# Kernel optimization log

Hardware: AMD Instinct MI355X
Metric: run time of the kernel (lower is better)

The kernel has to match this reference:

```python
import jax, jax.numpy as jnp
from jax import lax
import numpy as np

EPS = 1e-5


def ref_points(Hk, Wk):
    # torch linspace(0.5, Hk-0.5, Hk)/Hk * 2 - 1, stacked (y, x)
    ys = (jnp.linspace(0.5, Hk - 0.5, Hk) / Hk) * 2.0 - 1.0
    xs = (jnp.linspace(0.5, Wk - 0.5, Wk) / Wk) * 2.0 - 1.0
    yy, xx = jnp.meshgrid(ys, xs, indexing='ij')
    return jnp.stack([yy, xx], axis=-1)  # (Hk, Wk, 2) in (y, x) order


def grid_sample(img, grid):
    # Bilinear, align_corners=True, zeros padding (torch F.grid_sample defaults).
    # img: (N, C, Hi, Wi); grid: (N, Hg, Wg, 2) with (x, y) in [-1, 1].
    N, C, Hi, Wi = img.shape
    Hg, Wg = grid.shape[1], grid.shape[2]
    gx = (grid[..., 0] + 1.0) * 0.5 * (Wi - 1)
    gy = (grid[..., 1] + 1.0) * 0.5 * (Hi - 1)
    x0 = jnp.floor(gx)
    y0 = jnp.floor(gy)
    wx1 = gx - x0
    wy1 = gy - y0
    imgf = img.reshape(N, C, Hi * Wi)

    def corner(ix, iy, w):
        valid = (ix >= 0) & (ix < Wi) & (iy >= 0) & (iy < Hi)
        idx = (jnp.clip(iy, 0, Hi - 1).astype(jnp.int32) * Wi
               + jnp.clip(ix, 0, Wi - 1).astype(jnp.int32)).reshape(N, -1)
        vals = jax.vmap(lambda im, f: im[:, f])(imgf, idx)  # (N, C, Hg*Wg)
        return vals * (w * valid).reshape(N, 1, -1)

    out = (corner(x0, y0, (1 - wx1) * (1 - wy1))
           + corner(x0 + 1, y0, wx1 * (1 - wy1))
           + corner(x0, y0 + 1, (1 - wx1) * wy1)
           + corner(x0 + 1, y0 + 1, wx1 * wy1))
    return out.reshape(N, C, Hg, Wg)


def setup_inputs() -> dict:
    key = jax.random.key(0)
    ks = jax.random.split(key, 8)
    B, C, H, W = 8, 128, 64, 64
    gc, nH = 64, 4
    return {
        'x': jax.random.normal(ks[0], (B, C, H, W), jnp.float32),
        'w_dw': jax.random.normal(ks[1], (gc, 1, 5, 5), jnp.float32) * 0.1,
        'ln_w': jnp.ones((gc,), jnp.float32),
        'w_off': jax.random.normal(ks[2], (3, gc), jnp.float32) * 0.1,
        'wq': jax.random.normal(ks[3], (C, C), jnp.float32) * 0.05,
        'wk': jax.random.normal(ks[4], (C, C), jnp.float32) * 0.05,
        'wv': jax.random.normal(ks[5], (C, C), jnp.float32) * 0.05,
        'wo': jax.random.normal(ks[6], (C, C), jnp.float32) * 0.05,
        'rpe': jax.random.normal(ks[7], (nH, 2 * H - 1, 2 * W - 1), jnp.float32) * 0.01,
    }


def reference(x, w_dw, ln_w, w_off, wq, wk, wv, wo, rpe):
    B, C, H, W = x.shape
    G, nH = 2, 4
    gc = C // G           # group channels
    dh = C // nH          # head channels
    gh = nH // G          # heads per group
    scale = dh ** -0.5
    orf = 1.0             # offset_range_factor

    conv1x1 = lambda t, w: jnp.einsum('oi,bihw->bohw', w, t)

    q = conv1x1(x, wq)                                    # (B, C, H, W)
    q_off = q.reshape(B * G, gc, H, W)

    # conv_offset: depthwise 5x5 stride 4 pad 2 -> BiasFree LN (over C) -> GELU -> 1x1 to 3
    off = lax.conv_general_dilated(q_off, w_dw, (4, 4), ((2, 2), (2, 2)),
                                   dimension_numbers=('NCHW', 'OIHW', 'NCHW'),
                                   feature_group_count=gc)  # (B*G, gc, Hk, Wk)
    var = jnp.var(off, axis=1, keepdims=True)
    off = off / jnp.sqrt(var + EPS) * ln_w.reshape(1, -1, 1, 1)
    off = jax.nn.gelu(off, approximate=False)
    off = jnp.einsum('oi,bihw->bohw', w_off, off)          # (B*G, 3, Hk, Wk)

    Hk, Wk = off.shape[2], off.shape[3]
    n = Hk * Wk

    # channel 0 = y offset, channel 1 = x offset, channel 2 = modulation
    offset = jnp.stack([jnp.tanh(off[:, 0]) * (orf / Hk),
                        jnp.tanh(off[:, 1]) * (orf / Wk)], axis=-1)  # (B*G, Hk, Wk, 2) (y,x)
    dm = jax.nn.sigmoid(off[:, 2])[:, None]                # (B*G, 1, Hk, Wk)

    pos = offset + ref_points(Hk, Wk)[None]                # (B*G, Hk, Wk, 2) (y,x)

    xs = grid_sample(x.reshape(B * G, gc, H, W), pos[..., ::-1])  # grid in (x,y)
    xs = (xs * dm).reshape(B, C, 1, n)

    k = conv1x1(xs, wk).reshape(B * nH, dh, n)
    v = conv1x1(xs, wv).reshape(B * nH, dh, n)
    qf = q.reshape(B * nH, dh, H * W)

    attn = jnp.einsum('bcm,bcn->bmn', qf, k) * scale       # (B*nH, H*W, n)

    # relative-position bias sampled at continuous displacements
    rpe_b = jnp.broadcast_to(rpe[None], (B, nH, 2 * H - 1, 2 * W - 1)
                             ).reshape(B * G, gh, 2 * H - 1, 2 * W - 1)
    qg = ref_points(H, W).reshape(H * W, 2)                # (H*W, 2)
    disp = (qg[None, :, None, :] - pos.reshape(B * G, 1, n, 2)) * 0.5  # (B*G, H*W, n, 2)
    bias = grid_sample(rpe_b, disp[..., ::-1]).reshape(B * nH, H * W, n)

    attn = jax.nn.softmax(attn + bias, axis=2)
    out = jnp.einsum('bmn,bcn->bcm', attn, v).reshape(B, C, H, W)
    return conv1x1(out, wo)
```

## Files before the change

### kernel.cpp

```cpp
#include <hip/hip_runtime.h>
#include <hip/hip_bf16.h>
#include <math.h>

#define HW 4096
#define NCH 128

typedef __attribute__((ext_vector_type(8))) short short8;
typedef __attribute__((ext_vector_type(4))) float f32x4;

__device__ __forceinline__ short f2bf(float f) {
  union { __hip_bfloat16 h; short s; } u;
  u.h = __float2bfloat16(f);
  return u.s;
}
__device__ __forceinline__ float bf2f(short s) {
  union { unsigned u; float f; } u;
  u.u = ((unsigned)(unsigned short)s) << 16;
  return u.f;
}

__global__ __launch_bounds__(256) void xq_kernel(
    const float* __restrict__ x, const float* __restrict__ wq,
    short* __restrict__ xT, float* __restrict__ qT, short* __restrict__ qbf) {
  __shared__ float s[128][33];
  int tid = threadIdx.x;
  int b = blockIdx.y;
  int m0 = blockIdx.x * 32;
  {
    int ml = tid & 31, c0 = tid >> 5;
#pragma unroll
    for (int i = 0; i < 16; ++i) {
      int c = i * 8 + c0;
      s[c][ml] = x[((size_t)(b * NCH + c)) * HW + m0 + ml];
    }
  }
  __syncthreads();
  {
    int c = tid & 127, mh = tid >> 7;
#pragma unroll
    for (int i = 0; i < 16; ++i) {
      int m = i * 2 + mh;
      xT[((size_t)(b * HW + m0 + m)) * NCH + c] = f2bf(s[c][m]);
    }
  }
  int w = tid >> 6, lane = tid & 63, l15 = lane & 15, qd = lane >> 4;
  int mt = w & 1, og = w >> 1;
  int mrow = mt * 16 + l15;
  f32x4 acc[4];
#pragma unroll
  for (int oi = 0; oi < 4; ++oi) acc[oi] = (f32x4){0.f, 0.f, 0.f, 0.f};
#pragma unroll
  for (int kc = 0; kc < 4; ++kc) {
    short8 ah, al;
#pragma unroll
    for (int j = 0; j < 8; ++j) {
      float v = s[kc * 32 + qd * 8 + j][mrow];
      short hi = f2bf(v);
      ah[j] = hi;
      al[j] = f2bf(v - bf2f(hi));
    }
#pragma unroll
    for (int oi = 0; oi < 4; ++oi) {
      const float* wr =
          wq + (size_t)((og * 4 + oi) * 16 + l15) * NCH + kc * 32 + qd * 8;
      f32x4 w0 = *(const f32x4*)wr;
      f32x4 w1 = *(const f32x4*)(wr + 4);
      short8 bh, bl;
#pragma unroll
      for (int j = 0; j < 4; ++j) {
        short h0 = f2bf(w0[j]);
        bh[j] = h0;
        bl[j] = f2bf(w0[j] - bf2f(h0));
        short h1 = f2bf(w1[j]);
        bh[4 + j] = h1;
        bl[4 + j] = f2bf(w1[j] - bf2f(h1));
      }
      acc[oi] = __builtin_amdgcn_mfma_f32_16x16x32_bf16(ah, bh, acc[oi], 0, 0, 0);
      acc[oi] = __builtin_amdgcn_mfma_f32_16x16x32_bf16(al, bh, acc[oi], 0, 0, 0);
      acc[oi] = __builtin_amdgcn_mfma_f32_16x16x32_bf16(ah, bl, acc[oi], 0, 0, 0);
    }
  }
#pragma unroll
  for (int oi = 0; oi < 4; ++oi)
#pragma unroll
    for (int r = 0; r < 4; ++r) {
      size_t idx = ((size_t)(b * HW + m0 + mt * 16 + qd * 4 + r)) * NCH +
                   og * 64 + oi * 16 + l15;
      qT[idx] = acc[oi][r];
      qbf[idx] = f2bf(acc[oi][r]);
    }
}

__device__ __forceinline__ float wsum64(float v) {
#pragma unroll
  for (int o = 32; o > 0; o >>= 1) v += __shfl_xor(v, o);
  return v;
}

__global__ __launch_bounds__(256) void conv_offset_kernel(
    const float* __restrict__ qT, const float* __restrict__ w_dw,
    const float* __restrict__ ln_w, const float* __restrict__ w_off,
    const float* __restrict__ wk, const float* __restrict__ wv,
    const float* __restrict__ wo, const float* __restrict__ rpe,
    float* __restrict__ pos, float* __restrict__ dm,
    short* __restrict__ wk_bf, short* __restrict__ wv_bf,
    short* __restrict__ wo_bf, unsigned* __restrict__ tab) {
  int tid = threadIdx.x;
  if (blockIdx.x >= 64) {
    int id = (blockIdx.x - 64) * 16 + blockIdx.y;
    if (id < 64) {
      int i = id * 256 + tid;
      wk_bf[i] = f2bf(wk[i]);
      wv_bf[i] = f2bf(wv[i]);
      wo_bf[i] = f2bf(wo[i]);
    } else {
      int i = (id - 64) * 256 + tid;
      int h = i >> 14, r = i & 16383;
      int row = r >> 7, col = r & 127;
      float lo = 0.f, hi = 0.f;
      if (col < 127) {
        if (row >= 1) lo = rpe[h * 16129 + (row - 1) * 127 + col];
        if (row < 127) hi = rpe[h * 16129 + row * 127 + col];
      }
      union { unsigned u; _Float16 h2[2]; } pk;
      pk.h2[0] = (_Float16)lo;
      pk.h2[1] = (_Float16)hi;
      tab[i] = pk.u;
    }
    return;
  }
  int c = tid & 63;
  int p = blockIdx.x * 4 + (tid >> 6);
  int bg = blockIdx.y;
  int py = p >> 4, px = p & 15;
  const float* qp = qT + (size_t)(bg >> 1) * HW * NCH + (bg & 1) * 64 + c;
  const float* wd = w_dw + c * 25;
  float acc = 0.f;
#pragma unroll
  for (int ky = 0; ky < 5; ++ky) {
    int iy = 4 * py + ky - 2;
    if (iy < 0 || iy >= 64) continue;
#pragma unroll
    for (int kx = 0; kx < 5; ++kx) {
      int ix = 4 * px + kx - 2;
      if (ix < 0 || ix >= 64) continue;
      acc += wd[ky * 5 + kx] * qp[(size_t)(iy * 64 + ix) * NCH];
    }
  }
  float mean = wsum64(acc) * (1.f / 64.f);
  float msq = wsum64(acc * acc) * (1.f / 64.f);
  float var = msq - mean * mean;
  float g = acc * rsqrtf(var + 1e-5f) * ln_w[c];
  g = 0.5f * g * (1.f + erff(g * 0.70710678118654752f));
  float o0 = wsum64(w_off[c] * g);
  float o1 = wsum64(w_off[64 + c] * g);
  float o2 = wsum64(w_off[128 + c] * g);
  if (c == 0) {
    int idx = bg * 256 + p;
    pos[idx * 2] = tanhf(o0) * (1.f / 16.f) + ((py + 0.5f) * (1.f / 8.f) - 1.f);
    pos[idx * 2 + 1] = tanhf(o1) * (1.f / 16.f) + ((px + 0.5f) * (1.f / 8.f) - 1.f);
    dm[idx] = 1.f / (1.f + expf(-o2));
  }
}

__global__ __launch_bounds__(256) void sample_xs_kernel(
    const short* __restrict__ xT, const float* __restrict__ pos,
    const float* __restrict__ dm, short* __restrict__ xsT) {
  int tid = threadIdx.x;
  int c = tid & 63;
  int p = blockIdx.y * 4 + (tid >> 6);
  int bg = blockIdx.x;
  int b = bg >> 1, ch0 = (bg & 1) * 64;
  int idx = bg * 256 + p;
  float posy = pos[idx * 2], posx = pos[idx * 2 + 1];
  float dmv = dm[idx];
  float gx = (posx + 1.f) * 31.5f;
  float gy = (posy + 1.f) * 31.5f;
  float x0f = floorf(gx), y0f = floorf(gy);
  int ix = (int)x0f, iy = (int)y0f;
  float fx = gx - x0f, fy = gy - y0f;
  float w00 = (1.f - fx) * (1.f - fy), w10 = fx * (1.f - fy);
  float w01 = (1.f - fx) * fy, w11 = fx * fy;
  bool vx0 = (ix >= 0 && ix < 64), vx1 = (ix + 1 >= 0 && ix + 1 < 64);
  bool vy0 = (iy >= 0 && iy < 64), vy1 = (iy + 1 >= 0 && iy + 1 < 64);
  if (!(vx0 && vy0)) w00 = 0.f;
  if (!(vx1 && vy0)) w10 = 0.f;
  if (!(vx0 && vy1)) w01 = 0.f;
  if (!(vx1 && vy1)) w11 = 0.f;
  int x0c = min(max(ix, 0), 63), x1c = min(max(ix + 1, 0), 63);
  int y0c = min(max(iy, 0), 63), y1c = min(max(iy + 1, 0), 63);
  size_t rb = (size_t)b * HW * NCH + ch0 + c;
  float v = w00 * bf2f(xT[rb + (size_t)(y0c * 64 + x0c) * NCH]) +
            w10 * bf2f(xT[rb + (size_t)(y0c * 64 + x1c) * NCH]) +
            w01 * bf2f(xT[rb + (size_t)(y1c * 64 + x0c) * NCH]) +
            w11 * bf2f(xT[rb + (size_t)(y1c * 64 + x1c) * NCH]);
  xsT[((size_t)(b * 256 + p)) * NCH + ch0 + c] = f2bf(v * dmv);
}

__global__ __launch_bounds__(256) void kv_mfma_kernel(
    const short* __restrict__ xsT, const short* __restrict__ wk_bf,
    const short* __restrict__ wv_bf, short* __restrict__ kbf,
    short* __restrict__ vbf) {
  int tid = threadIdx.x;
  int w = tid >> 6, lane = tid & 63, l15 = lane & 15, qd = lane >> 4;
  int bh = blockIdx.x, b = bh >> 2;
  int n0 = blockIdx.y * 64 + w * 16;
  int ot = blockIdx.z & 1;
  f32x4 acc = (f32x4){0.f, 0.f, 0.f, 0.f};

  size_t xrow = ((size_t)(b * 256 + n0 + l15)) * NCH + qd * 8;
  size_t wrow = (size_t)((bh & 3) * 32 + ot * 16 + l15) * NCH + qd * 8;
  if ((blockIdx.z & 2) == 0) {
#pragma unroll
    for (int kc = 0; kc < 4; ++kc) {
      short8 a = *(const short8*)&xsT[xrow + kc * 32];
      short8 bb = *(const short8*)&wk_bf[wrow + kc * 32];
      acc = __builtin_amdgcn_mfma_f32_16x16x32_bf16(a, bb, acc, 0, 0, 0);
    }
#pragma unroll
    for (int r = 0; r < 4; ++r)
      kbf[((size_t)(bh * 256 + n0 + qd * 4 + r)) * 32 + ot * 16 + l15] =
          f2bf(acc[r]);
  } else {
#pragma unroll
    for (int kc = 0; kc < 4; ++kc) {
      short8 bb = *(const short8*)&xsT[xrow + kc * 32];
      short8 a = *(const short8*)&wv_bf[wrow + kc * 32];
      acc = __builtin_amdgcn_mfma_f32_16x16x32_bf16(a, bb, acc, 0, 0, 0);
    }
#pragma unroll
    for (int r = 0; r < 4; ++r)
      vbf[((size_t)(bh * 32 + ot * 16 + qd * 4 + r)) * 256 + n0 + l15] =
          f2bf(acc[r]);
  }
}

#define PROW 264
#define TROWS 72

__global__ __launch_bounds__(256) void attn_kernel(
    const short* __restrict__ qbf, const short* __restrict__ kbf,
    const short* __restrict__ vbf, const float* __restrict__ pos,
    const unsigned* __restrict__ tabg, short* __restrict__ outT) {
  __shared__ __align__(16) unsigned s_tab[TROWS * 128];
  __shared__ __align__(16) float s_pos[512];
  short* s_p = (short*)s_tab;

  int tid = threadIdx.x;
  int wv = tid >> 6;
  int lane = tid & 63;
  int l15 = lane & 15;
  int qd = lane >> 4;
  int bh = blockIdx.y;
  int b = bh >> 2, h = bh & 3;
  int bg = b * 2 + (h >> 1);
  int m0 = blockIdx.x * 64 + wv * 16;

  float ry = ((float)blockIdx.x + 0.5f) * (1.f / 32.f) - 1.f;
  float gy0 = 63.f + ry * 31.5f;
  int row0 = min(max((int)floorf(gy0) - 34, 0), 128 - TROWS);

  {
    const uint4* src = (const uint4*)(tabg + (size_t)h * 16384 + row0 * 128);
    uint4* dst = (uint4*)s_tab;
#pragma unroll
    for (int i = 0; i < 9; ++i) dst[i * 256 + tid] = src[i * 256 + tid];
    const float* posg = pos + (size_t)bg * 512;
    s_pos[tid] = posg[tid];
    s_pos[256 + tid] = posg[256 + tid];
  }

  short8 qfrag =
      *(const short8*)&qbf[((size_t)(b * HW + m0 + l15)) * NCH + h * 32 + qd * 8];

  f32x4 acc[16];
  {
    const short* kb = kbf + ((size_t)bh * 256 + l15) * 32 + qd * 8;
#pragma unroll
    for (int t = 0; t < 16; ++t) {
      short8 kf = *(const short8*)(kb + t * 16 * 32);
      acc[t] = __builtin_amdgcn_mfma_f32_16x16x32_bf16(
          kf, qfrag, (f32x4){0.f, 0.f, 0.f, 0.f}, 0, 0, 0);
    }
  }
  __syncthreads();

  int m = m0 + l15;
  float gx0 = ((((float)(m & 63) + 0.5f) * (1.f / 32.f) - 1.f) * 0.5f + 1.f) * 63.f;
  float gyb = gy0 - (float)row0 + 1.f;
  float mxA[4] = {-1e30f, -1e30f, -1e30f, -1e30f};
#pragma unroll
  for (int t = 0; t < 16; ++t) {
    const f32x4* pp4 = (const f32x4*)&s_pos[(t * 16 + qd * 4) * 2];
    f32x4 pA = pp4[0];
    f32x4 pB = pp4[1];
    float py[4] = {pA[0], pA[2], pB[0], pB[2]};
    float px[4] = {pA[1], pA[3], pB[1], pB[3]};
#pragma unroll
    for (int r = 0; r < 4; ++r) {
      float gy = gyb - py[r] * 31.5f;
      float gx = gx0 - px[r] * 31.5f;
      float y0f = floorf(gy), x0f = floorf(gx);
      float fy = gy - y0f, fx = gx - x0f;
      int row = (int)y0f << 7;
      int xl = (int)x0f;
      unsigned left = s_tab[row + (xl & 127)];
      unsigned right = s_tab[row + xl + 1];
      union { unsigned u; _Float16 h2[2]; } L, R;
      L.u = left;
      R.u = right;
      float t00 = (float)L.h2[0], t01 = (float)L.h2[1];
      float t10 = (float)R.h2[0], t11 = (float)R.h2[1];
      float r0 = t00 + fx * (t10 - t00);
      float r1 = t01 + fx * (t11 - t01);
      float bias = r0 + fy * (r1 - r0);
      float s = fmaf(acc[t][r], 0.17677669529663688f, bias);
      acc[t][r] = s;
      mxA[r] = fmaxf(mxA[r], s);
    }
  }
  float mx = fmaxf(fmaxf(mxA[0], mxA[1]), fmaxf(mxA[2], mxA[3]));
  mx = fmaxf(mx, __shfl_xor(mx, 16));
  float M = fmaxf(mx, __shfl_xor(mx, 32));

  float smA[4] = {0.f, 0.f, 0.f, 0.f};
#pragma unroll
  for (int t = 0; t < 16; ++t) {
#pragma unroll
    for (int r = 0; r < 4; ++r) {
      float e = __expf(acc[t][r] - M);
      acc[t][r] = e;
      smA[r] += e;
    }
  }
  float sm = (smA[0] + smA[1]) + (smA[2] + smA[3]);
  sm += __shfl_xor(sm, 16);
  sm += __shfl_xor(sm, 32);
  float inv = 1.f / sm;

  __syncthreads();

  {
    short* pw = s_p + wv * 16 * PROW + l15 * PROW;
#pragma unroll
    for (int t = 0; t < 16; ++t) {
      int n = t * 16 + qd * 4;
      short4 pk;
      pk.x = f2bf(acc[t][0]);
      pk.y = f2bf(acc[t][1]);
      pk.z = f2bf(acc[t][2]);
      pk.w = f2bf(acc[t][3]);
      *(short4*)(pw + n) = pk;
    }
  }

  f32x4 o0 = {0.f, 0.f, 0.f, 0.f}, o1 = {0.f, 0.f, 0.f, 0.f};
  {
    const short* vb = vbf + ((size_t)bh * 32 + l15) * 256 + qd * 8;
    const short* pr = s_p + wv * 16 * PROW + l15 * PROW + qd * 8;
#pragma unroll
    for (int ch = 0; ch < 8; ++ch) {
      short8 pf = *(const short8*)(pr + ch * 32);
      short8 v0 = *(const short8*)(vb + ch * 32);
      short8 v1 = *(const short8*)(vb + 16 * 256 + ch * 32);
      o0 = __builtin_amdgcn_mfma_f32_16x16x32_bf16(v0, pf, o0, 0, 0, 0);
      o1 = __builtin_amdgcn_mfma_f32_16x16x32_bf16(v1, pf, o1, 0, 0, 0);
    }
  }
  {
    size_t row = (size_t)(b * HW + m0 + l15) * NCH + h * 32 + qd * 4;
    short4 s0, s1;
    s0.x = f2bf(o0[0] * inv); s0.y = f2bf(o0[1] * inv);
    s0.z = f2bf(o0[2] * inv); s0.w = f2bf(o0[3] * inv);
    s1.x = f2bf(o1[0] * inv); s1.y = f2bf(o1[1] * inv);
    s1.z = f2bf(o1[2] * inv); s1.w = f2bf(o1[3] * inv);
    *(short4*)&outT[row] = s0;
    *(short4*)&outT[row + 16] = s1;
  }
}

__global__ __launch_bounds__(256) void wo_mfma_kernel(
    const short* __restrict__ attnT, const short* __restrict__ wo_bf,
    float* __restrict__ out) {
  int tid = threadIdx.x;
  int wv = tid >> 6;
  int lane = tid & 63;
  int l15 = lane & 15;
  int qd = lane >> 4;
  int b = blockIdx.x >> 6;
  int m0 = (blockIdx.x & 63) * 64 + wv * 16;

  f32x4 acc[8];
#pragma unroll
  for (int ot = 0; ot < 8; ++ot) acc[ot] = (f32x4){0.f, 0.f, 0.f, 0.f};

  const short* arow = attnT + (size_t)(b * HW + m0 + l15) * NCH + qd * 8;
  const short* wrow = wo_bf + (size_t)l15 * NCH + qd * 8;
#pragma unroll
  for (int kc = 0; kc < 4; ++kc) {
    short8 afrag = *(const short8*)(arow + kc * 32);
#pragma unroll
    for (int ot = 0; ot < 8; ++ot) {
      short8 bfrag = *(const short8*)(wrow + (size_t)ot * 16 * NCH + kc * 32);
      acc[ot] = __builtin_amdgcn_mfma_f32_16x16x32_bf16(afrag, bfrag, acc[ot],
                                                        0, 0, 0);
    }
  }
#pragma unroll
  for (int ot = 0; ot < 8; ++ot) {
    float* op = out + ((size_t)b * NCH + ot * 16 + l15) * HW + m0 + qd * 4;
    *(f32x4*)op = acc[ot];
  }
}

extern "C" void kernel_launch(void* const* d_in, const int* in_sizes, int n_in,
                              void* d_out, int out_size, void* d_ws,
                              size_t ws_size, hipStream_t stream) {
  const float* x = (const float*)d_in[0];
  const float* w_dw = (const float*)d_in[1];
  const float* ln_w = (const float*)d_in[2];
  const float* w_off = (const float*)d_in[3];
  const float* wq = (const float*)d_in[4];
  const float* wk = (const float*)d_in[5];
  const float* wv = (const float*)d_in[6];
  const float* wo = (const float*)d_in[7];
  const float* rpe = (const float*)d_in[8];
  float* out = (float*)d_out;

  float* qT = out;
  short* sb = (short*)d_ws;
  short* xT = sb;
  short* outT = sb;
  short* xsT = sb + 4194304;
  short* kbf = sb + 4456448;
  short* vbf = sb + 4718592;
  short* wk_bf = sb + 4980736;
  short* wv_bf = sb + 4997120;
  short* wo_bf = sb + 5013504;
  unsigned* tab = (unsigned*)(sb + 5029888);
  float* pos = (float*)(sb + 5160960);
  float* dm = pos + 8192;
  short* qbf = sb + 5185536;

  xq_kernel<<<dim3(128, 8), 256, 0, stream>>>(x, wq, xT, qT, qbf);
  conv_offset_kernel<<<dim3(84, 16), 256, 0, stream>>>(
      qT, w_dw, ln_w, w_off, wk, wv, wo, rpe, pos, dm, wk_bf, wv_bf, wo_bf,
      tab);
  sample_xs_kernel<<<dim3(16, 64), 256, 0, stream>>>(xT, pos, dm, xsT);
  kv_mfma_kernel<<<dim3(32, 4, 4), 256, 0, stream>>>(xsT, wk_bf, wv_bf, kbf,
                                                     vbf);
  attn_kernel<<<dim3(64, 32), 256, 0, stream>>>(qbf, kbf, vbf, pos, tab, outT);
  wo_mfma_kernel<<<512, 256, 0, stream>>>(outT, wo_bf, out);
}
```

Before: 184.2 us.

## Fuse deformable sampling into offset kernel and software-pipeline bias table loads

Merges the separate sample_xs kernel into the offset-computation kernel so each thread samples x directly using its freshly computed position and modulation, dropping the dm buffer and a kernel launch. The bf16 copy of q is no longer written in xq_kernel; attn_kernel instead reads fp32 q and converts it to bf16 in registers. The attention bias loop is double-buffered so LDS table lookups for the next tile are issued before the current tile's interpolation runs, and attn_kernel gets a launch_bounds occupancy hint. This trades extra register pressure and wider q reads in attention for fewer launches and less global traffic.

Measured after the change: 194.9 us. 5.8% more time.

```diff
diff --git a/kernel.cpp b/kernel.cpp
--- a/kernel.cpp
+++ b/kernel.cpp
@@ -21,7 +21,7 @@
 
 __global__ __launch_bounds__(256) void xq_kernel(
     const float* __restrict__ x, const float* __restrict__ wq,
-    short* __restrict__ xT, float* __restrict__ qT, short* __restrict__ qbf) {
+    short* __restrict__ xT, float* __restrict__ qT) {
   __shared__ float s[128][33];
   int tid = threadIdx.x;
   int b = blockIdx.y;
@@ -83,12 +83,9 @@
 #pragma unroll
   for (int oi = 0; oi < 4; ++oi)
 #pragma unroll
-    for (int r = 0; r < 4; ++r) {
-      size_t idx = ((size_t)(b * HW + m0 + mt * 16 + qd * 4 + r)) * NCH +
-                   og * 64 + oi * 16 + l15;
-      qT[idx] = acc[oi][r];
-      qbf[idx] = f2bf(acc[oi][r]);
-    }
+    for (int r = 0; r < 4; ++r)
+      qT[((size_t)(b * HW + m0 + mt * 16 + qd * 4 + r)) * NCH + og * 64 +
+         oi * 16 + l15] = acc[oi][r];
 }
 
 __device__ __forceinline__ float wsum64(float v) {
@@ -97,14 +94,15 @@
   return v;
 }
 
-__global__ __launch_bounds__(256) void conv_offset_kernel(
+__global__ __launch_bounds__(256) void offs_kernel(
     const float* __restrict__ qT, const float* __restrict__ w_dw,
     const float* __restrict__ ln_w, const float* __restrict__ w_off,
-    const float* __restrict__ wk, const float* __restrict__ wv,
-    const float* __restrict__ wo, const float* __restrict__ rpe,
-    float* __restrict__ pos, float* __restrict__ dm,
-    short* __restrict__ wk_bf, short* __restrict__ wv_bf,
-    short* __restrict__ wo_bf, unsigned* __restrict__ tab) {
+    const short* __restrict__ xT, const float* __restrict__ wk,
+    const float* __restrict__ wv, const float* __restrict__ wo,
+    const float* __restrict__ rpe, float* __restrict__ pos,
+    short* __restrict__ xsT, short* __restrict__ wk_bf,
+    short* __restrict__ wv_bf, short* __restrict__ wo_bf,
+    unsigned* __restrict__ tab) {
   int tid = threadIdx.x;
   if (blockIdx.x >= 64) {
     int id = (blockIdx.x - 64) * 16 + blockIdx.y;
@@ -133,7 +131,8 @@
   int p = blockIdx.x * 4 + (tid >> 6);
   int bg = blockIdx.y;
   int py = p >> 4, px = p & 15;
-  const float* qp = qT + (size_t)(bg >> 1) * HW * NCH + (bg & 1) * 64 + c;
+  int b = bg >> 1, ch0 = (bg & 1) * 64;
+  const float* qp = qT + (size_t)b * HW * NCH + ch0 + c;
   const float* wd = w_dw + c * 25;
   float acc = 0.f;
 #pragma unroll
@@ -155,25 +154,14 @@
   float o0 = wsum64(w_off[c] * g);
   float o1 = wsum64(w_off[64 + c] * g);
   float o2 = wsum64(w_off[128 + c] * g);
+  float posy = tanhf(o0) * (1.f / 16.f) + ((py + 0.5f) * (1.f / 8.f) - 1.f);
+  float posx = tanhf(o1) * (1.f / 16.f) + ((px + 0.5f) * (1.f / 8.f) - 1.f);
+  float dmv = 1.f / (1.f + expf(-o2));
   if (c == 0) {
     int idx = bg * 256 + p;
-    pos[idx * 2] = tanhf(o0) * (1.f / 16.f) + ((py + 0.5f) * (1.f / 8.f) - 1.f);
-    pos[idx * 2 + 1] = tanhf(o1) * (1.f / 16.f) + ((px + 0.5f) * (1.f / 8.f) - 1.f);
-    dm[idx] = 1.f / (1.f + expf(-o2));
-  }
-}
-
-__global__ __launch_bounds__(256) void sample_xs_kernel(
-    const short* __restrict__ xT, const float* __restrict__ pos,
-    const float* __restrict__ dm, short* __restrict__ xsT) {
-  int tid = threadIdx.x;
-  int c = tid & 63;
-  int p = blockIdx.y * 4 + (tid >> 6);
-  int bg = blockIdx.x;
-  int b = bg >> 1, ch0 = (bg & 1) * 64;
-  int idx = bg * 256 + p;
-  float posy = pos[idx * 2], posx = pos[idx * 2 + 1];
-  float dmv = dm[idx];
+    pos[idx * 2] = posy;
+    pos[idx * 2 + 1] = posx;
+  }
   float gx = (posx + 1.f) * 31.5f;
   float gy = (posy + 1.f) * 31.5f;
   float x0f = floorf(gx), y0f = floorf(gy);
@@ -238,8 +226,8 @@
 #define PROW 264
 #define TROWS 72
 
-__global__ __launch_bounds__(256) void attn_kernel(
-    const short* __restrict__ qbf, const short* __restrict__ kbf,
+__global__ __launch_bounds__(256, 4) void attn_kernel(
+    const float* __restrict__ qT, const short* __restrict__ kbf,
     const short* __restrict__ vbf, const float* __restrict__ pos,
     const unsigned* __restrict__ tabg, short* __restrict__ outT) {
   __shared__ __align__(16) unsigned s_tab[TROWS * 128];
@@ -270,8 +258,17 @@
     s_pos[256 + tid] = posg[256 + tid];
   }
 
-  short8 qfrag =
-      *(const short8*)&qbf[((size_t)(b * HW + m0 + l15)) * NCH + h * 32 + qd * 8];
+  short8 qfrag;
+  {
+    const float* qg = qT + ((size_t)(b * HW + m0 + l15)) * NCH + h * 32 + qd * 8;
+    f32x4 a0 = *(const f32x4*)qg;
+    f32x4 a1 = *(const f32x4*)(qg + 4);
+#pragma unroll
+    for (int j = 0; j < 4; ++j) {
+      qfrag[j] = f2bf(a0[j]);
+      qfrag[4 + j] = f2bf(a1[j]);
+    }
+  }
 
   f32x4 acc[16];
   {
@@ -288,29 +285,43 @@
   int m = m0 + l15;
   float gx0 = ((((float)(m & 63) + 0.5f) * (1.f / 32.f) - 1.f) * 0.5f + 1.f) * 63.f;
   float gyb = gy0 - (float)row0 + 1.f;
-  float mxA[4] = {-1e30f, -1e30f, -1e30f, -1e30f};
-#pragma unroll
-  for (int t = 0; t < 16; ++t) {
+
+  float fxS[2][4], fyS[2][4];
+  unsigned LS[2][4], RS[2][4];
+  auto load_stage = [&](int sidx, int t) {
     const f32x4* pp4 = (const f32x4*)&s_pos[(t * 16 + qd * 4) * 2];
     f32x4 pA = pp4[0];
     f32x4 pB = pp4[1];
-    float py[4] = {pA[0], pA[2], pB[0], pB[2]};
-    float px[4] = {pA[1], pA[3], pB[1], pB[3]};
+    float pyv[4] = {pA[0], pA[2], pB[0], pB[2]};
+    float pxv[4] = {pA[1], pA[3], pB[1], pB[3]};
 #pragma unroll
     for (int r = 0; r < 4; ++r) {
-      float gy = gyb - py[r] * 31.5f;
-      float gx = gx0 - px[r] * 31.5f;
+      float gy = gyb - pyv[r] * 31.5f;
+      float gx = gx0 - pxv[r] * 31.5f;
       float y0f = floorf(gy), x0f = floorf(gx);
-      float fy = gy - y0f, fx = gx - x0f;
+      fyS[sidx][r] = gy - y0f;
+      fxS[sidx][r] = gx - x0f;
       int row = (int)y0f << 7;
       int xl = (int)x0f;
-      unsigned left = s_tab[row + (xl & 127)];
-      unsigned right = s_tab[row + xl + 1];
+      LS[sidx][r] = s_tab[row + (xl & 127)];
+      RS[sidx][r] = s_tab[row + xl + 1];
+    }
+  };
+
+  load_stage(0, 0);
+  float mxA[4] = {-1e30f, -1e30f, -1e30f, -1e30f};
+#pragma unroll
+  for (int t = 0; t < 16; ++t) {
+    int cur = t & 1;
+    if (t < 15) load_stage(cur ^ 1, t + 1);
+#pragma unroll
+    for (int r = 0; r < 4; ++r) {
       union { unsigned u; _Float16 h2[2]; } L, R;
-      L.u = left;
-      R.u = right;
+      L.u = LS[cur][r];
+      R.u = RS[cur][r];
       float t00 = (float)L.h2[0], t01 = (float)L.h2[1];
       float t10 = (float)R.h2[0], t11 = (float)R.h2[1];
+      float fx = fxS[cur][r], fy = fyS[cur][r];
       float r0 = t00 + fx * (t10 - t00);
       float r1 = t01 + fx * (t11 - t01);
       float bias = r0 + fy * (r1 - r0);
@@ -439,16 +450,13 @@
   short* wo_bf = sb + 5013504;
   unsigned* tab = (unsigned*)(sb + 5029888);
   float* pos = (float*)(sb + 5160960);
-  float* dm = pos + 8192;
-  short* qbf = sb + 5185536;
-
-  xq_kernel<<<dim3(128, 8), 256, 0, stream>>>(x, wq, xT, qT, qbf);
-  conv_offset_kernel<<<dim3(84, 16), 256, 0, stream>>>(
-      qT, w_dw, ln_w, w_off, wk, wv, wo, rpe, pos, dm, wk_bf, wv_bf, wo_bf,
-      tab);
-  sample_xs_kernel<<<dim3(16, 64), 256, 0, stream>>>(xT, pos, dm, xsT);
+
+  xq_kernel<<<dim3(128, 8), 256, 0, stream>>>(x, wq, xT, qT);
+  offs_kernel<<<dim3(84, 16), 256, 0, stream>>>(qT, w_dw, ln_w, w_off, xT, wk,
+                                                wv, wo, rpe, pos, xsT, wk_bf,
+                                                wv_bf, wo_bf, tab);
   kv_mfma_kernel<<<dim3(32, 4, 4), 256, 0, stream>>>(xsT, wk_bf, wv_bf, kbf,
                                                      vbf);
-  attn_kernel<<<dim3(64, 32), 256, 0, stream>>>(qbf, kbf, vbf, pos, tab, outT);
+  attn_kernel<<<dim3(64, 32), 256, 0, stream>>>(qT, kbf, vbf, pos, tab, outT);
   wo_mfma_kernel<<<512, 256, 0, stream>>>(outT, wo_bf, out);
 }
```
